# Kernel tuning notes

Hardware: AMD Instinct MI355X
Metric: run time of the kernel (lower is better)

The kernel has to match this reference:

```python
import jax, jax.numpy as jnp
import numpy as np

H, D_HEAD, MEM, K_OUT, J_DIM = 4, 16, 64, 192, 256
LN_EPS = 1e-5

def setup_inputs() -> dict:
    key = jax.random.key(0)
    ks = jax.random.split(key, 12)
    B, T, P = 4, 2048, 16
    inp = {
        "joint_repr": jax.random.normal(ks[0], (B, T, P, J_DIM), jnp.float32),
        "curvature": jax.random.uniform(ks[1], (B,), jnp.float32),
        "entropy": jax.random.uniform(ks[2], (B,), jnp.float32),
        "Wq": 0.02 * jax.random.normal(ks[3], (MEM, J_DIM), jnp.float32),
        "Wk": 0.02 * jax.random.normal(ks[4], (MEM, J_DIM), jnp.float32),
        "Wv": 0.02 * jax.random.normal(ks[5], (MEM, J_DIM), jnp.float32),
        "Wbeta_w": 0.05 * jax.random.normal(ks[6], (H, J_DIM), jnp.float32),
        "Wbeta_b": jnp.full((H,), 0.5, jnp.float32),
        "Walpha_w": 0.05 * jax.random.normal(ks[7], (H, J_DIM), jnp.float32),
        "Walpha_b": jnp.full((H,), -1.0, jnp.float32),
        "curv_w": 0.001 * jax.random.normal(ks[8], (H, 1), jnp.float32),
        "ent_w": 0.001 * jax.random.normal(ks[9], (H, 1), jnp.float32),
        "out_w": 0.01 * jax.random.normal(ks[10], (K_OUT, MEM), jnp.float32),
        "out_b": jnp.zeros((K_OUT,), jnp.float32),
        "ln_q_w": jnp.ones((D_HEAD,), jnp.float32),
        "ln_q_b": jnp.zeros((D_HEAD,), jnp.float32),
        "ln_k_w": jnp.ones((D_HEAD,), jnp.float32),
        "ln_k_b": jnp.zeros((D_HEAD,), jnp.float32),
    }
    return inp

def _ln(y, w, b):
    m = jnp.mean(y, axis=-1, keepdims=True)
    var = jnp.mean((y - m) ** 2, axis=-1, keepdims=True)
    return (y - m) / jnp.sqrt(var + LN_EPS) * w + b

def reference(joint_repr, curvature, entropy, Wq, Wk, Wv, Wbeta_w, Wbeta_b,
              Walpha_w, Walpha_b, curv_w, ent_w, out_w, out_b,
              ln_q_w, ln_q_b, ln_k_w, ln_k_b):
    B, T, P, J = joint_repr.shape
    N = B * P
    x = joint_repr.reshape(N, T, J)  # matches torch reshape(B*P, T, J)
    q = _ln((x @ Wq.T).reshape(N, T, H, D_HEAD), ln_q_w, ln_q_b)
    k = _ln((x @ Wk.T).reshape(N, T, H, D_HEAD), ln_k_w, ln_k_b)
    v = (x @ Wv.T).reshape(N, T, H, D_HEAD)
    k = k / jnp.clip(jnp.linalg.norm(k, axis=-1, keepdims=True), 1e-12)
    beta = jax.nn.sigmoid(x @ Wbeta_w.T + Wbeta_b)    # (N,T,H)
    alpha = jax.nn.sigmoid(x @ Walpha_w.T + Walpha_b)  # (N,T,H)
    # curvature modulation (detached in original)
    Kv = jnp.clip(jnp.abs(jax.lax.stop_gradient(curvature)), None, 10.0)
    Kv = jnp.repeat(Kv, P)  # (N,)
    beta = jax.nn.sigmoid(beta + Kv[:, None, None] * curv_w[:, 0])
    # entropy modulation (detached)
    Sv = jnp.clip(jax.lax.stop_gradient(entropy), 0.0, 5.0)
    Sv = jnp.repeat(Sv, P)
    alpha = jax.nn.sigmoid(alpha + Sv[:, None, None] * ent_w[:, 0])

    def step(M, inps):
        k_t, v_t, q_t, b_t, a_t = inps  # (N,H,d), (N,H)
        Mk = jnp.einsum('nhij,nhj->nhi', M, k_t)
        outer_kk = Mk[..., :, None] * k_t[..., None, :]
        outer_vk = v_t[..., :, None] * k_t[..., None, :]
        M = M - a_t[:, :, None, None] * outer_kk + b_t[:, :, None, None] * outer_vk
        o = jnp.einsum('nhij,nhj->nhi', M, q_t)
        return M, o

    M0 = jnp.zeros((N, H, D_HEAD, D_HEAD), joint_repr.dtype)
    xs = (k.transpose(1, 0, 2, 3), v.transpose(1, 0, 2, 3), q.transpose(1, 0, 2, 3),
          beta.transpose(1, 0, 2), alpha.transpose(1, 0, 2))
    _, outs = jax.lax.scan(step, M0, xs)  # (T,N,H,d)
    out = outs.transpose(1, 0, 2, 3).reshape(N, T, H * D_HEAD)
    fib = out @ out_w.T + out_b  # (N,T,K)
    return fib.reshape(B, P, T, K_OUT).transpose(0, 2, 1, 3)  # (B,T,P,K)
```

## Files before the change

### kernel.cpp

```cpp
#include <hip/hip_runtime.h>

#define TDIM 2048
#define SEG 16
#define SEGLEN 128

typedef __attribute__((ext_vector_type(8))) short short8;
typedef __attribute__((ext_vector_type(4))) short short4v;
typedef __attribute__((ext_vector_type(4))) float float4v;

__device__ __forceinline__ float sigf(float x) { return 1.0f / (1.0f + __expf(-x)); }

__device__ __forceinline__ unsigned short f2bf_rne(float f) {
    unsigned u = __float_as_uint(f);
    unsigned r = (u + 0x7fffu + ((u >> 16) & 1u)) >> 16;
    return (unsigned short)r;
}
__device__ __forceinline__ float bf2f(unsigned short h) {
    return __uint_as_float(((unsigned)h) << 16);
}
struct bfpair { short hi, lo; };
__device__ __forceinline__ bfpair cvt_split(float x) {
    bfpair p;
    unsigned short h = f2bf_rne(x);
    p.hi = (short)h;
    p.lo = (short)f2bf_rne(x - bf2f(h));
    return p;
}
__device__ __forceinline__ void split4(float4 v, short4v& hi, short4v& lo) {
    bfpair a = cvt_split(v.x), b = cvt_split(v.y), c = cvt_split(v.z), d = cvt_split(v.w);
    short4v h = {a.hi, b.hi, c.hi, d.hi};
    short4v l = {a.lo, b.lo, c.lo, d.lo};
    hi = h; lo = l;
}

#define RED16(v) { v += __shfl_xor(v, 1); v += __shfl_xor(v, 2); \
                   v += __shfl_xor(v, 4); v += __shfl_xor(v, 8); }

__device__ __forceinline__ float dot4f(float4 a, float4 b) {
    return fmaf(a.w, b.w, fmaf(a.z, b.z, fmaf(a.y, b.y, a.x * b.x)));
}
__device__ __forceinline__ float red4g(float v) {
    v += __shfl_xor(v, 16);
    v += __shfl_xor(v, 32);
    return v;
}

#define LROW 136

__global__ __launch_bounds__(256) void prep_w_kernel(
    const float* __restrict__ Wq, const float* __restrict__ Wk, const float* __restrict__ Wv,
    const float* __restrict__ Wbw, const float* __restrict__ Waw,
    short* __restrict__ wimg)
{
    int u = blockIdx.x * 256 + threadIdx.x;
    if (u >= 6656) return;
    int kc = u / 1664, rem = u % 1664;
    int rr = rem >> 3, gg = rem & 7;
    const float* wrow = nullptr;
    if (rr < 64)       wrow = Wq  + (size_t)rr * 256;
    else if (rr < 128) wrow = Wk  + (size_t)(rr - 64) * 256;
    else if (rr < 192) wrow = Wv  + (size_t)(rr - 128) * 256;
    else if (rr < 196) wrow = Wbw + (size_t)(rr - 192) * 256;
    else if (rr < 200) wrow = Waw + (size_t)(rr - 196) * 256;
    short* dst = wimg + (size_t)u * 16;
#pragma unroll
    for (int s = 0; s < 8; ++s) {
        float v = wrow ? wrow[kc * 64 + gg * 8 + s] : 0.0f;
        bfpair p = cvt_split(v);
        dst[s] = p.hi; dst[8 + s] = p.lo;
    }
}

__global__ __launch_bounds__(256) void prep_ow_kernel(
    const float* __restrict__ ow, short* __restrict__ owimg)
{
    int u = blockIdx.x * 256 + threadIdx.x;
    if (u >= 1536) return;
    int rr = u >> 3, gg = u & 7;
    short* dst = owimg + (size_t)u * 16;
#pragma unroll
    for (int s = 0; s < 8; ++s) {
        bfpair p = cvt_split(ow[(size_t)rr * 64 + gg * 8 + s]);
        dst[s] = p.hi; dst[8 + s] = p.lo;
    }
}

__global__ __launch_bounds__(256, 2) void proj_kernel(
    const float* __restrict__ x, const float* __restrict__ curv, const float* __restrict__ ent,
    const short* __restrict__ wimg,
    const float* __restrict__ Wbb, const float* __restrict__ Wab,
    const float* __restrict__ cw, const float* __restrict__ ew,
    const float* __restrict__ lnqw, const float* __restrict__ lnqb,
    const float* __restrict__ lnkw, const float* __restrict__ lnkb,
    float* __restrict__ q_ws, float* __restrict__ k_ws, float* __restrict__ v_ws,
    float* __restrict__ beta_ws, float* __restrict__ alpha_ws)
{
    __shared__ __align__(16) short xsh[64 * LROW];
    __shared__ __align__(16) short wsh[208 * LROW];

    const int tid = threadIdx.x;
    const int lane = tid & 63, wv = tid >> 6;
    const int row0 = blockIdx.x * 64;

    float4v acc[13];
#pragma unroll
    for (int cc = 0; cc < 13; ++cc) acc[cc] = (float4v){0.f, 0.f, 0.f, 0.f};

    for (int kc = 0; kc < 4; ++kc) {
        __syncthreads();
#pragma unroll
        for (int it = 0; it < 4; ++it) {
            int f = it * 256 + tid;
            int rr = f >> 4, c4 = f & 15;
            float4 xv = *(const float4*)&x[(size_t)(row0 + rr) * 256 + kc * 64 + c4 * 4];
            short4v hi, lo;
            split4(xv, hi, lo);
            short* ph = &xsh[rr * LROW + (c4 >> 1) * 16 + (c4 & 1) * 4];
            *(short4v*)ph = hi;
            *(short4v*)(ph + 8) = lo;
        }
        {
            const int4* wsrc = (const int4*)(wimg + (size_t)kc * 26624);
#pragma unroll
            for (int it = 0; it < 13; ++it) {
                int f = it * 256 + tid;
                int4 tv = wsrc[f];
                int row = f >> 4, idx = f & 15;
                *(int4*)&wsh[row * LROW + (idx >> 1) * 16 + (idx & 1) * 8] = tv;
            }
        }
        __syncthreads();
#pragma unroll
        for (int ks = 0; ks < 2; ++ks) {
            const int rowA = wv * 16 + (lane & 15);
            const int g4 = ks * 4 + (lane >> 4);
            short8 ah = *(const short8*)&xsh[rowA * LROW + g4 * 16];
            short8 al = *(const short8*)&xsh[rowA * LROW + g4 * 16 + 8];
#pragma unroll
            for (int nt = 0; nt < 13; ++nt) {
                const int rowB = nt * 16 + (lane & 15);
                short8 bh = *(const short8*)&wsh[rowB * LROW + g4 * 16];
                short8 bl = *(const short8*)&wsh[rowB * LROW + g4 * 16 + 8];
                acc[nt] = __builtin_amdgcn_mfma_f32_16x16x32_bf16(ah, bh, acc[nt], 0, 0, 0);
                acc[nt] = __builtin_amdgcn_mfma_f32_16x16x32_bf16(ah, bl, acc[nt], 0, 0, 0);
                acc[nt] = __builtin_amdgcn_mfma_f32_16x16x32_bf16(al, bh, acc[nt], 0, 0, 0);
            }
        }
    }

    const int c = lane & 15, lq = lane >> 4;
    const float lnqw_c = lnqw[c], lnqb_c = lnqb[c];
    const float lnkw_c = lnkw[c], lnkb_c = lnkb[c];
#pragma unroll
    for (int j = 0; j < 4; ++j) {
        const int grow = row0 + wv * 16 + lq * 4 + j;
        const int n = grow >> 11, t = grow & 2047;
#pragma unroll
        for (int h = 0; h < 4; ++h) {
            float y = acc[h][j];
            float s = y;  RED16(s);
            float s2 = y * y;  RED16(s2);
            float mean = s * 0.0625f;
            float var = s2 * 0.0625f - mean * mean;
            float inv = rsqrtf(var + 1e-5f);
            q_ws[((size_t)(n * 4 + h) * TDIM + t) * 16 + c] = (y - mean) * inv * lnqw_c + lnqb_c;
        }
#pragma unroll
        for (int h = 0; h < 4; ++h) {
            float y = acc[4 + h][j];
            float s = y;  RED16(s);
            float s2 = y * y;  RED16(s2);
            float mean = s * 0.0625f;
            float var = s2 * 0.0625f - mean * mean;
            float inv = rsqrtf(var + 1e-5f);
            float kn = (y - mean) * inv * lnkw_c + lnkb_c;
            float s3 = kn * kn;  RED16(s3);
            kn = kn / fmaxf(sqrtf(s3), 1e-12f);
            k_ws[((size_t)(n * 4 + h) * TDIM + t) * 16 + c] = kn;
        }
#pragma unroll
        for (int h = 0; h < 4; ++h)
            v_ws[((size_t)(n * 4 + h) * TDIM + t) * 16 + c] = acc[8 + h][j];
        float yb = acc[12][j];
        if (c < 4) {
            float Kv = fminf(fabsf(curv[n >> 4]), 10.0f);
            beta_ws[(size_t)(n * 4 + c) * TDIM + t] = sigf(sigf(yb + Wbb[c]) + Kv * cw[c]);
        } else if (c < 8) {
            int h = c - 4;
            float Sv = fminf(fmaxf(ent[n >> 4], 0.0f), 5.0f);
            alpha_ws[(size_t)(n * 4 + h) * TDIM + t] = sigf(sigf(yb + Wab[h]) + Sv * ew[h]);
        }
    }
}


__global__ __launch_bounds__(64) void scan_p1_kernel(
    const float* __restrict__ k_ws, const float* __restrict__ v_ws,
    const float* __restrict__ beta_ws, const float* __restrict__ alpha_ws,
    float* __restrict__ pq_ws)
{
    __shared__ __align__(16) float ks[128 * 16], bvs[128 * 16];
    __shared__ __align__(16) float tb1[128 * 4];
    const int tid = threadIdx.x;
    const int sid = blockIdx.x;
    const int cid = blockIdx.y;
    const int i = tid & 15, g = tid >> 4;
    const int t0g = sid * SEGLEN;
    const float* kb = k_ws + ((size_t)cid * TDIM + t0g) * 16;
    const float* vb = v_ws + ((size_t)cid * TDIM + t0g) * 16;
    const float* bb = beta_ws + (size_t)cid * TDIM + t0g;
    const float* ab = alpha_ws + (size_t)cid * TDIM + t0g;

    for (int f = tid; f < 128 * 16; f += 64) { ks[f] = 0.f; bvs[f] = 0.f; }
    for (int f = tid; f < 128 * 4; f += 64) tb1[f] = 0.f;
    __syncthreads();

    float4 kr[4], vr[4]; float be = 0.f, alp = 0.f;
    auto load_stage = [&](int s) {
        size_t t0 = (size_t)s * 64 + tid;
        const float4* kp = (const float4*)(kb + t0 * 16);
        const float4* vp = (const float4*)(vb + t0 * 16);
#pragma unroll
        for (int j = 0; j < 4; ++j) { kr[j] = kp[j]; vr[j] = vp[j]; }
        be = bb[t0]; alp = ab[t0];
    };
    auto commit_stage = [&](int s) {
        int r = (s & 1) * 64 + tid;
#pragma unroll
        for (int j = 0; j < 4; ++j) {
            *(float4*)&ks[r * 16 + 4 * j] = kr[j];
            float4 bv4 = make_float4(be * vr[j].x, be * vr[j].y, be * vr[j].z, be * vr[j].w);
            *(float4*)&bvs[r * 16 + 4 * j] = bv4;
        }
    };
    auto table_pass = [&](int s) {
        int r0 = (s & 1) * 64 + tid;
        int rm1 = (r0 - 1) & 127, rm2 = (r0 - 2) & 127;
        float C = 0.f, C2 = 0.f;
#pragma unroll
        for (int j = 0; j < 4; ++j) {
            float4 kt  = *(float4*)&ks[r0 * 16 + 4 * j];
            float4 km1 = *(float4*)&ks[rm1 * 16 + 4 * j];
            float4 km2 = *(float4*)&ks[rm2 * 16 + 4 * j];
            C  += dot4f(km1, kt);
            C2 += dot4f(km2, kt);
        }
        *(float4*)&tb1[r0 * 4] = make_float4(alp * C, alp * C2, alp, 0.f);
    };

    load_stage(0);
    commit_stage(0);
    __syncthreads();
    table_pass(0);
    __syncthreads();

    float4 Q4 = make_float4(0.f, 0.f, 0.f, 0.f);
    float4 P4 = make_float4(i == 4 * g + 0 ? 1.f : 0.f,
                            i == 4 * g + 1 ? 1.f : 0.f,
                            i == 4 * g + 2 ? 1.f : 0.f,
                            i == 4 * g + 3 ? 1.f : 0.f);
    float wq1 = 0.f, wq2 = 0.f, wp1 = 0.f, wp2 = 0.f;
    float4 k4m1 = make_float4(0.f, 0.f, 0.f, 0.f);
    float4 k4_0 = *(float4*)&ks[0 * 16 + 4 * g];
    float4 k4p1 = *(float4*)&ks[1 * 16 + 4 * g];
    float upQ_cur = 0.f;
    float upP_cur = ks[i];
    float4 ta0 = *(float4*)&tb1[0];
    float aC1_c = ta0.x, aC2_c = ta0.y, al_c = ta0.z;
    float bv_c = bvs[i];

    int t = 0;
    auto step = [&]() {
        int rp2 = (t + 2) & 127, rp1 = (t + 1) & 127;
        float4 k4in = *(float4*)&ks[rp2 * 16 + 4 * g];
        float4 tain = *(float4*)&tb1[rp1 * 4];
        float bvin = bvs[rp1 * 16 + i];
        float upQ = red4g(dot4f(Q4, k4p1));
        float upP = red4g(dot4f(P4, k4p1));
        Q4.x = fmaf(wq1, k4m1.x, Q4.x);
        Q4.y = fmaf(wq1, k4m1.y, Q4.y);
        Q4.z = fmaf(wq1, k4m1.z, Q4.z);
        Q4.w = fmaf(wq1, k4m1.w, Q4.w);
        P4.x = fmaf(wp1, k4m1.x, P4.x);
        P4.y = fmaf(wp1, k4m1.y, P4.y);
        P4.z = fmaf(wp1, k4m1.z, P4.z);
        P4.w = fmaf(wp1, k4m1.w, P4.w);
        float rq = fmaf(-aC2_c, wq2, fmaf(-al_c, upQ_cur, bv_c));
        float wq0 = fmaf(-aC1_c, wq1, rq);
        float rp_ = fmaf(-aC2_c, wp2, -al_c * upP_cur);
        float wp0 = fmaf(-aC1_c, wp1, rp_);
        wq2 = wq1; wq1 = wq0; wp2 = wp1; wp1 = wp0;
        k4m1 = k4_0; k4_0 = k4p1; k4p1 = k4in;
        upQ_cur = upQ; upP_cur = upP;
        aC1_c = tain.x; aC2_c = tain.y; al_c = tain.z; bv_c = bvin;
        ++t;
    };

    load_stage(1);
#pragma unroll 4
    for (int u = 0; u < 32; ++u) step();
    commit_stage(1);
#pragma unroll 4
    for (int u = 0; u < 16; ++u) step();
    table_pass(1);
#pragma unroll 4
    for (int u = 0; u < 16; ++u) step();
#pragma unroll 4
    for (int u = 0; u < 64; ++u) step();

    Q4.x = fmaf(wq1, k4m1.x, Q4.x);
    Q4.y = fmaf(wq1, k4m1.y, Q4.y);
    Q4.z = fmaf(wq1, k4m1.z, Q4.z);
    Q4.w = fmaf(wq1, k4m1.w, Q4.w);
    P4.x = fmaf(wp1, k4m1.x, P4.x);
    P4.y = fmaf(wp1, k4m1.y, P4.y);
    P4.z = fmaf(wp1, k4m1.z, P4.z);
    P4.w = fmaf(wp1, k4m1.w, P4.w);

    float* dst = pq_ws + ((size_t)cid * 15 + sid) * 512;
    *(float4*)&dst[i * 16 + 4 * g] = Q4;
    *(float4*)&dst[256 + i * 16 + 4 * g] = P4;
}

__global__ __launch_bounds__(64) void scan_p2_kernel(
    const float* __restrict__ pq_ws, float* __restrict__ min_ws)
{
    __shared__ float Mlds[256], Plds[256];
    const int tid = threadIdx.x;
    const int cid = blockIdx.x;
    const int i = tid & 15, g = tid >> 4;
    float4 M4 = make_float4(0.f, 0.f, 0.f, 0.f);
    *(float4*)&min_ws[((size_t)cid * SEG + 0) * 256 + i * 16 + 4 * g] = M4;
    for (int sid = 0; sid < 15; ++sid) {
        const float* base = pq_ws + ((size_t)cid * 15 + sid) * 512;
        float4 Qn = *(const float4*)&base[i * 16 + 4 * g];
        float4 Pn = *(const float4*)&base[256 + i * 16 + 4 * g];
        *(float4*)&Mlds[i * 16 + 4 * g] = M4;
        *(float4*)&Plds[i * 16 + 4 * g] = Pn;
        __syncthreads();
        float4 acc = Qn;
#pragma unroll
        for (int m = 0; m < 16; ++m) {
            float mm = Mlds[i * 16 + m];
            float4 pr = *(float4*)&Plds[m * 16 + 4 * g];
            acc.x = fmaf(mm, pr.x, acc.x);
            acc.y = fmaf(mm, pr.y, acc.y);
            acc.z = fmaf(mm, pr.z, acc.z);
            acc.w = fmaf(mm, pr.w, acc.w);
        }
        M4 = acc;
        __syncthreads();
        *(float4*)&min_ws[((size_t)cid * SEG + sid + 1) * 256 + i * 16 + 4 * g] = M4;
    }
}

__global__ __launch_bounds__(64) void scan_p3_kernel(
    const float* __restrict__ q_ws, const float* __restrict__ k_ws, const float* __restrict__ v_ws,
    const float* __restrict__ beta_ws, const float* __restrict__ alpha_ws,
    const float* __restrict__ min_ws, float* __restrict__ o_ws)
{
    __shared__ __align__(16) float ks[128 * 16], qs[128 * 16], bvs[128 * 16];
    __shared__ __align__(16) float tbl[128 * 8];
    __shared__ __align__(16) float os[64 * 16];
    const int tid = threadIdx.x;
    const int sid = blockIdx.x;
    const int cid = blockIdx.y;
    const int i = tid & 15, g = tid >> 4;
    const int t0g = sid * SEGLEN;
    const float* kb = k_ws + ((size_t)cid * TDIM + t0g) * 16;
    const float* qb = q_ws + ((size_t)cid * TDIM + t0g) * 16;
    const float* vb = v_ws + ((size_t)cid * TDIM + t0g) * 16;
    const float* bb = beta_ws + (size_t)cid * TDIM + t0g;
    const float* ab = alpha_ws + (size_t)cid * TDIM + t0g;
    float* obp = o_ws + ((size_t)cid * TDIM + t0g) * 16;

    for (int f = tid; f < 128 * 16; f += 64) { ks[f] = 0.f; qs[f] = 0.f; bvs[f] = 0.f; }
    for (int f = tid; f < 128 * 8; f += 64) tbl[f] = 0.f;
    __syncthreads();

    float4 kr[4], qr[4], vr[4]; float be = 0.f, alp = 0.f;
    auto load_stage = [&](int s) {
        size_t t0 = (size_t)s * 64 + tid;
        const float4* kp = (const float4*)(kb + t0 * 16);
        const float4* qp = (const float4*)(qb + t0 * 16);
        const float4* vp = (const float4*)(vb + t0 * 16);
#pragma unroll
        for (int j = 0; j < 4; ++j) { kr[j] = kp[j]; qr[j] = qp[j]; vr[j] = vp[j]; }
        be = bb[t0]; alp = ab[t0];
    };
    auto commit_stage = [&](int s) {
        int r = (s & 1) * 64 + tid;
#pragma unroll
        for (int j = 0; j < 4; ++j) {
            *(float4*)&ks[r * 16 + 4 * j] = kr[j];
            *(float4*)&qs[r * 16 + 4 * j] = qr[j];
            float4 bv4 = make_float4(be * vr[j].x, be * vr[j].y, be * vr[j].z, be * vr[j].w);
            *(float4*)&bvs[r * 16 + 4 * j] = bv4;
        }
    };
    auto table_pass = [&](int s) {
        int r0 = (s & 1) * 64 + tid;
        int rm1 = (r0 - 1) & 127, rm2 = (r0 - 2) & 127;
        float C = 0.f, C2 = 0.f, d = 0.f, e = 0.f, E2 = 0.f;
#pragma unroll
        for (int j = 0; j < 4; ++j) {
            float4 kt  = *(float4*)&ks[r0 * 16 + 4 * j];
            float4 km1 = *(float4*)&ks[rm1 * 16 + 4 * j];
            float4 km2 = *(float4*)&ks[rm2 * 16 + 4 * j];
            float4 qt  = *(float4*)&qs[r0 * 16 + 4 * j];
            C  += dot4f(km1, kt);
            C2 += dot4f(km2, kt);
            d  += dot4f(kt,  qt);
            e  += dot4f(km1, qt);
            E2 += dot4f(km2, qt);
        }
        *(float4*)&tbl[r0 * 8] = make_float4(alp * C, alp * C2, d, e);
        *(float2*)&tbl[r0 * 8 + 4] = make_float2(E2, alp);
    };

    load_stage(0);
    commit_stage(0);
    __syncthreads();
    table_pass(0);
    __syncthreads();

    float4 M4 = *(const float4*)&min_ws[((size_t)cid * SEG + sid) * 256 + i * 16 + 4 * g];
    float w1 = 0.f, w2 = 0.f;
    float4 k4m1 = make_float4(0.f, 0.f, 0.f, 0.f);
    float4 k4_0 = *(float4*)&ks[0 * 16 + 4 * g];
    float4 q4_0 = *(float4*)&qs[0 * 16 + 4 * g];
    float4 k4p1 = *(float4*)&ks[1 * 16 + 4 * g];
    float4 q4p1 = *(float4*)&qs[1 * 16 + 4 * g];
    float up_cur = red4g(dot4f(M4, k4_0));
    float rp_cur = red4g(dot4f(M4, q4_0));
    float4 ta0 = *(float4*)&tbl[0];
    float aC1_c = ta0.x, aC2_c = ta0.y, d_c = ta0.z, e_c = ta0.w;
    float2 tx0 = *(float2*)&tbl[4];
    float E2_c = tx0.x, al_c = tx0.y;
    float bv_c = bvs[i];

    int t = 0;
    auto step = [&]() {
        int rp2 = (t + 2) & 127, rp1 = (t + 1) & 127;
        float4 k4in = *(float4*)&ks[rp2 * 16 + 4 * g];
        float4 q4in = *(float4*)&qs[rp2 * 16 + 4 * g];
        float4 tain = *(float4*)&tbl[rp1 * 8];
        float2 txin = *(float2*)&tbl[rp1 * 8 + 4];
        float bvin = bvs[rp1 * 16 + i];
        float up = red4g(dot4f(M4, k4p1));
        float rp = red4g(dot4f(M4, q4p1));
        M4.x = fmaf(w1, k4m1.x, M4.x);
        M4.y = fmaf(w1, k4m1.y, M4.y);
        M4.z = fmaf(w1, k4m1.z, M4.z);
        M4.w = fmaf(w1, k4m1.w, M4.w);
        float r = fmaf(-aC2_c, w2, fmaf(-al_c, up_cur, bv_c));
        float w0 = fmaf(-aC1_c, w1, r);
        float o = fmaf(w0, d_c, fmaf(w1, e_c, fmaf(w2, E2_c, rp_cur)));
        if (g == 0) os[(t & 63) * 16 + i] = o;
        w2 = w1; w1 = w0;
        k4m1 = k4_0; k4_0 = k4p1; k4p1 = k4in;
        q4p1 = q4in;
        up_cur = up; rp_cur = rp;
        aC1_c = tain.x; aC2_c = tain.y; d_c = tain.z; e_c = tain.w;
        E2_c = txin.x; al_c = txin.y; bv_c = bvin;
        ++t;
    };

    for (int s = 0; s < 2; ++s) {
        if (s == 0) load_stage(1);
#pragma unroll 4
        for (int u = 0; u < 32; ++u) step();
        if (s == 0) commit_stage(1);
#pragma unroll 4
        for (int u = 0; u < 16; ++u) step();
        if (s == 0) table_pass(1);
#pragma unroll 4
        for (int u = 0; u < 16; ++u) step();
#pragma unroll
        for (int j = 0; j < 4; ++j) {
            float4 ov = *(float4*)&os[(tid * 4 + j) * 4];
            *(float4*)&obp[(size_t)s * 1024 + (tid * 4 + j) * 4] = ov;
        }
    }
}

__global__ __launch_bounds__(256, 2) void outproj_kernel(
    const float* __restrict__ o_ws, const short* __restrict__ owimg,
    const float* __restrict__ ob, float* __restrict__ out)
{
    __shared__ __align__(16) short osh[64 * LROW];
    __shared__ __align__(16) short wsh[192 * LROW];
    const int tid = threadIdx.x;
    const int lane = tid & 63, wv = tid >> 6;
    const int row0 = blockIdx.x * 64;

    float4v acc[12];
#pragma unroll
    for (int cc = 0; cc < 12; ++cc) acc[cc] = (float4v){0.f, 0.f, 0.f, 0.f};

#pragma unroll
    for (int it = 0; it < 4; ++it) {
        int f = it * 256 + tid;
        int rr = f >> 4, c4 = f & 15;
        int grow = row0 + rr;
        int n = grow >> 11, t = grow & 2047;
        int h = c4 >> 2, d4 = c4 & 3;
        float4 xv = *(const float4*)&o_ws[((size_t)(n * 4 + h) * TDIM + t) * 16 + d4 * 4];
        short4v hi, lo;
        split4(xv, hi, lo);
        short* ph = &osh[rr * LROW + (c4 >> 1) * 16 + (c4 & 1) * 4];
        *(short4v*)ph = hi;
        *(short4v*)(ph + 8) = lo;
    }
    {
        const int4* wsrc = (const int4*)owimg;
#pragma unroll
        for (int it = 0; it < 12; ++it) {
            int f = it * 256 + tid;
            int4 tv = wsrc[f];
            int row = f >> 4, idx = f & 15;
            *(int4*)&wsh[row * LROW + (idx >> 1) * 16 + (idx & 1) * 8] = tv;
        }
    }
    __syncthreads();

#pragma unroll
    for (int ks = 0; ks < 2; ++ks) {
        const int rowA = wv * 16 + (lane & 15);
        const int g4 = ks * 4 + (lane >> 4);
        short8 ah = *(const short8*)&osh[rowA * LROW + g4 * 16];
        short8 al = *(const short8*)&osh[rowA * LROW + g4 * 16 + 8];
#pragma unroll
        for (int nt = 0; nt < 12; ++nt) {
            const int rowB = nt * 16 + (lane & 15);
            short8 bh = *(const short8*)&wsh[rowB * LROW + g4 * 16];
            short8 bl = *(const short8*)&wsh[rowB * LROW + g4 * 16 + 8];
            acc[nt] = __builtin_amdgcn_mfma_f32_16x16x32_bf16(ah, bh, acc[nt], 0, 0, 0);
            acc[nt] = __builtin_amdgcn_mfma_f32_16x16x32_bf16(ah, bl, acc[nt], 0, 0, 0);
            acc[nt] = __builtin_amdgcn_mfma_f32_16x16x32_bf16(al, bh, acc[nt], 0, 0, 0);
        }
    }

    const int c = lane & 15, lq = lane >> 4;
#pragma unroll
    for (int nt = 0; nt < 12; ++nt) {
        float bias = ob[nt * 16 + c];
#pragma unroll
        for (int j = 0; j < 4; ++j) {
            int grow = row0 + wv * 16 + lq * 4 + j;
            int n = grow >> 11, t = grow & 2047;
            int b = n >> 4, p = n & 15;
            out[((size_t)(b * TDIM + t) * 16 + p) * 192 + nt * 16 + c] = acc[nt][j] + bias;
        }
    }
}

extern "C" void kernel_launch(void* const* d_in, const int* in_sizes, int n_in,
                              void* d_out, int out_size, void* d_ws, size_t ws_size,
                              hipStream_t stream) {
    (void)in_sizes; (void)n_in; (void)out_size; (void)ws_size;
    const float* x    = (const float*)d_in[0];
    const float* curv = (const float*)d_in[1];
    const float* ent  = (const float*)d_in[2];
    const float* Wq   = (const float*)d_in[3];
    const float* Wk   = (const float*)d_in[4];
    const float* Wv   = (const float*)d_in[5];
    const float* Wbw  = (const float*)d_in[6];
    const float* Wbb  = (const float*)d_in[7];
    const float* Waw  = (const float*)d_in[8];
    const float* Wab  = (const float*)d_in[9];
    const float* cw   = (const float*)d_in[10];
    const float* ew   = (const float*)d_in[11];
    const float* ow   = (const float*)d_in[12];
    const float* ob   = (const float*)d_in[13];
    const float* lnqw = (const float*)d_in[14];
    const float* lnqb = (const float*)d_in[15];
    const float* lnkw = (const float*)d_in[16];
    const float* lnkb = (const float*)d_in[17];
    float* out = (float*)d_out;

    float* ws = (float*)d_ws;
    float* q_ws     = ws;
    float* k_ws     = q_ws + 8388608;
    float* v_ws     = k_ws + 8388608;
    float* beta_ws  = v_ws + 8388608;
    float* alpha_ws = beta_ws + 524288;
    float* o_ws     = alpha_ws + 524288;

    short* wimg  = (short*)o_ws;
    short* owimg = (short*)q_ws;
    float* pq_ws  = out;
    float* min_ws = out + 1966080;

    prep_w_kernel<<<26, 256, 0, stream>>>(Wq, Wk, Wv, Wbw, Waw, wimg);
    proj_kernel<<<2048, 256, 0, stream>>>(x, curv, ent, wimg, Wbb, Wab,
                                          cw, ew, lnqw, lnqb, lnkw, lnkb,
                                          q_ws, k_ws, v_ws, beta_ws, alpha_ws);
    scan_p1_kernel<<<dim3(15, 256), 64, 0, stream>>>(k_ws, v_ws, beta_ws, alpha_ws, pq_ws);
    scan_p2_kernel<<<256, 64, 0, stream>>>(pq_ws, min_ws);
    scan_p3_kernel<<<dim3(16, 256), 64, 0, stream>>>(q_ws, k_ws, v_ws, beta_ws, alpha_ws,
                                                     min_ws, o_ws);
    prep_ow_kernel<<<6, 256, 0, stream>>>(ow, owimg);
    outproj_kernel<<<2048, 256, 0, stream>>>(o_ws, owimg, ob, out);
}
```

Before: 495.2 us.

## Restructure projection GEMMs with column-split waves, swizzled LDS, and direct global-to-LDS loads

The projection and output-projection GEMMs now split output columns across waves instead of rows, so each wave keeps A fragments for all 64 rows in registers and reuses them across its column tiles. LDS padding is replaced by an XOR swizzle baked into the prepacked weight images, and weights are copied with global_load_lds. The next x chunk is prefetched into registers while the current one is converted. Further changes are packed bf16 conversion via v_cvt_pk_bf16_f32 and DPP-based 16-lane reductions. These target LDS traffic, bank conflicts and load latency, at the cost of uneven work per wave (4 vs 3 tiles) and hand-written waitcnt handling.

```diff
diff --git a/kernel.cpp b/kernel.cpp
--- a/kernel.cpp
+++ b/kernel.cpp
@@ -26,15 +26,36 @@
     p.lo = (short)f2bf_rne(x - bf2f(h));
     return p;
 }
-__device__ __forceinline__ void split4(float4 v, short4v& hi, short4v& lo) {
-    bfpair a = cvt_split(v.x), b = cvt_split(v.y), c = cvt_split(v.z), d = cvt_split(v.w);
-    short4v h = {a.hi, b.hi, c.hi, d.hi};
-    short4v l = {a.lo, b.lo, c.lo, d.lo};
-    hi = h; lo = l;
-}
-
-#define RED16(v) { v += __shfl_xor(v, 1); v += __shfl_xor(v, 2); \
-                   v += __shfl_xor(v, 4); v += __shfl_xor(v, 8); }
+
+__device__ __forceinline__ void split4_fast(float4 v, short4v& hi, short4v& lo) {
+    unsigned h01, h23;
+    asm("v_cvt_pk_bf16_f32 %0, %1, %2" : "=v"(h01) : "v"(v.x), "v"(v.y));
+    asm("v_cvt_pk_bf16_f32 %0, %1, %2" : "=v"(h23) : "v"(v.z), "v"(v.w));
+    float rx = v.x - __uint_as_float(h01 << 16);
+    float ry = v.y - __uint_as_float(h01 & 0xffff0000u);
+    float rz = v.z - __uint_as_float(h23 << 16);
+    float rw = v.w - __uint_as_float(h23 & 0xffff0000u);
+    unsigned l01, l23;
+    asm("v_cvt_pk_bf16_f32 %0, %1, %2" : "=v"(l01) : "v"(rx), "v"(ry));
+    asm("v_cvt_pk_bf16_f32 %0, %1, %2" : "=v"(l23) : "v"(rz), "v"(rw));
+    union { unsigned u[2]; short4v s; } uh, ul;
+    uh.u[0] = h01; uh.u[1] = h23;
+    ul.u[0] = l01; ul.u[1] = l23;
+    hi = uh.s; lo = ul.s;
+}
+
+template<int CTRL>
+__device__ __forceinline__ float dpp_addt(float v) {
+    int t = __builtin_amdgcn_update_dpp(0, __float_as_int(v), CTRL, 0xf, 0xf, true);
+    return v + __int_as_float(t);
+}
+__device__ __forceinline__ float red16d(float v) {
+    v = dpp_addt<0xB1>(v);
+    v = dpp_addt<0x4E>(v);
+    v = dpp_addt<0x141>(v);
+    v = dpp_addt<0x140>(v);
+    return v;
+}
 
 __device__ __forceinline__ float dot4f(float4 a, float4 b) {
     return fmaf(a.w, b.w, fmaf(a.z, b.z, fmaf(a.y, b.y, a.x * b.x)));
@@ -45,7 +66,11 @@
     return v;
 }
 
-#define LROW 136
+__device__ __forceinline__ void gld16(const void* g, void* l) {
+    __builtin_amdgcn_global_load_lds(
+        (const __attribute__((address_space(1))) unsigned*)g,
+        (__attribute__((address_space(3))) unsigned*)l, 16, 0, 0);
+}
 
 __global__ __launch_bounds__(256) void prep_w_kernel(
     const float* __restrict__ Wq, const float* __restrict__ Wk, const float* __restrict__ Wv,
@@ -62,12 +87,14 @@
     else if (rr < 192) wrow = Wv  + (size_t)(rr - 128) * 256;
     else if (rr < 196) wrow = Wbw + (size_t)(rr - 192) * 256;
     else if (rr < 200) wrow = Waw + (size_t)(rr - 196) * 256;
-    short* dst = wimg + (size_t)u * 16;
+    int usw = (2 * gg) ^ (rr & 7);
+    short* dh = wimg + ((size_t)kc * 3328 + rr * 16 + usw) * 8;
+    short* dl = wimg + ((size_t)kc * 3328 + rr * 16 + (usw ^ 1)) * 8;
 #pragma unroll
     for (int s = 0; s < 8; ++s) {
         float v = wrow ? wrow[kc * 64 + gg * 8 + s] : 0.0f;
         bfpair p = cvt_split(v);
-        dst[s] = p.hi; dst[8 + s] = p.lo;
+        dh[s] = p.hi; dl[s] = p.lo;
     }
 }
 
@@ -77,11 +104,13 @@
     int u = blockIdx.x * 256 + threadIdx.x;
     if (u >= 1536) return;
     int rr = u >> 3, gg = u & 7;
-    short* dst = owimg + (size_t)u * 16;
+    int usw = (2 * gg) ^ (rr & 7);
+    short* dh = owimg + ((size_t)rr * 16 + usw) * 8;
+    short* dl = owimg + ((size_t)rr * 16 + (usw ^ 1)) * 8;
 #pragma unroll
     for (int s = 0; s < 8; ++s) {
         bfpair p = cvt_split(ow[(size_t)rr * 64 + gg * 8 + s]);
-        dst[s] = p.hi; dst[8 + s] = p.lo;
+        dh[s] = p.hi; dl[s] = p.lo;
     }
 }
 
@@ -95,104 +124,130 @@
     float* __restrict__ q_ws, float* __restrict__ k_ws, float* __restrict__ v_ws,
     float* __restrict__ beta_ws, float* __restrict__ alpha_ws)
 {
-    __shared__ __align__(16) short xsh[64 * LROW];
-    __shared__ __align__(16) short wsh[208 * LROW];
+    __shared__ __align__(16) short xsh[64 * 128];
+    __shared__ __align__(16) short wsh[208 * 128];
 
     const int tid = threadIdx.x;
     const int lane = tid & 63, wv = tid >> 6;
+    const int i16 = lane & 15, gq = lane >> 4, swz = i16 & 7;
     const int row0 = blockIdx.x * 64;
-
-    float4v acc[13];
-#pragma unroll
-    for (int cc = 0; cc < 13; ++cc) acc[cc] = (float4v){0.f, 0.f, 0.f, 0.f};
-
+    const int ntbase = (wv == 0) ? 0 : (1 + 3 * wv);
+    const int ntcnt  = (wv == 0) ? 4 : 3;
+
+    float4v acc[4][4];
+#pragma unroll
+    for (int m = 0; m < 4; ++m)
+#pragma unroll
+        for (int nI = 0; nI < 4; ++nI) acc[m][nI] = (float4v){0.f, 0.f, 0.f, 0.f};
+
+    float4 xr[4];
+#pragma unroll
+    for (int it = 0; it < 4; ++it) {
+        int f = it * 256 + tid, rr = f >> 4, c4 = f & 15;
+        xr[it] = *(const float4*)&x[(size_t)(row0 + rr) * 256 + c4 * 4];
+    }
+
+#pragma unroll
     for (int kc = 0; kc < 4; ++kc) {
-        __syncthreads();
+        __builtin_amdgcn_s_barrier();
+        const short* wsrc = wimg + (size_t)kc * 26624;
+#pragma unroll
+        for (int it = 0; it < 13; ++it) {
+            int f = it * 256 + tid;
+            gld16(wsrc + (size_t)f * 8, &wsh[f * 8]);
+        }
+        asm volatile("" ::: "memory");
 #pragma unroll
         for (int it = 0; it < 4; ++it) {
-            int f = it * 256 + tid;
-            int rr = f >> 4, c4 = f & 15;
-            float4 xv = *(const float4*)&x[(size_t)(row0 + rr) * 256 + kc * 64 + c4 * 4];
+            int f = it * 256 + tid, rr = f >> 4, c4 = f & 15;
             short4v hi, lo;
-            split4(xv, hi, lo);
-            short* ph = &xsh[rr * LROW + (c4 >> 1) * 16 + (c4 & 1) * 4];
-            *(short4v*)ph = hi;
-            *(short4v*)(ph + 8) = lo;
-        }
-        {
-            const int4* wsrc = (const int4*)(wimg + (size_t)kc * 26624);
-#pragma unroll
-            for (int it = 0; it < 13; ++it) {
-                int f = it * 256 + tid;
-                int4 tv = wsrc[f];
-                int row = f >> 4, idx = f & 15;
-                *(int4*)&wsh[row * LROW + (idx >> 1) * 16 + (idx & 1) * 8] = tv;
+            split4_fast(xr[it], hi, lo);
+            int usw = (2 * (c4 >> 1)) ^ (rr & 7);
+            *(short4v*)&xsh[rr * 128 + usw * 8 + (c4 & 1) * 4] = hi;
+            *(short4v*)&xsh[rr * 128 + (usw ^ 1) * 8 + (c4 & 1) * 4] = lo;
+        }
+        if (kc < 3) {
+#pragma unroll
+            for (int it = 0; it < 4; ++it) {
+                int f = it * 256 + tid, rr = f >> 4, c4 = f & 15;
+                xr[it] = *(const float4*)&x[(size_t)(row0 + rr) * 256 + (kc + 1) * 64 + c4 * 4];
             }
-        }
-        __syncthreads();
+            asm volatile("s_waitcnt vmcnt(4) lgkmcnt(0)" ::: "memory");
+        } else {
+            asm volatile("s_waitcnt vmcnt(0) lgkmcnt(0)" ::: "memory");
+        }
+        __builtin_amdgcn_s_barrier();
 #pragma unroll
         for (int ks = 0; ks < 2; ++ks) {
-            const int rowA = wv * 16 + (lane & 15);
-            const int g4 = ks * 4 + (lane >> 4);
-            short8 ah = *(const short8*)&xsh[rowA * LROW + g4 * 16];
-            short8 al = *(const short8*)&xsh[rowA * LROW + g4 * 16 + 8];
-#pragma unroll
-            for (int nt = 0; nt < 13; ++nt) {
-                const int rowB = nt * 16 + (lane & 15);
-                short8 bh = *(const short8*)&wsh[rowB * LROW + g4 * 16];
-                short8 bl = *(const short8*)&wsh[rowB * LROW + g4 * 16 + 8];
-                acc[nt] = __builtin_amdgcn_mfma_f32_16x16x32_bf16(ah, bh, acc[nt], 0, 0, 0);
-                acc[nt] = __builtin_amdgcn_mfma_f32_16x16x32_bf16(ah, bl, acc[nt], 0, 0, 0);
-                acc[nt] = __builtin_amdgcn_mfma_f32_16x16x32_bf16(al, bh, acc[nt], 0, 0, 0);
+            const int g4 = ks * 4 + gq;
+            const int uA = ((2 * g4) ^ swz) * 8;
+            short8 ah[4], al[4];
+#pragma unroll
+            for (int m = 0; m < 4; ++m) {
+                const int rb = (m * 16 + i16) * 128;
+                ah[m] = *(const short8*)&xsh[rb + uA];
+                al[m] = *(const short8*)&xsh[rb + (uA ^ 8)];
             }
-        }
-    }
-
-    const int c = lane & 15, lq = lane >> 4;
+#pragma unroll
+            for (int nI = 0; nI < 4; ++nI) if (nI < ntcnt) {
+                const int rowB = ((ntbase + nI) * 16 + i16) * 128;
+                short8 bh = *(const short8*)&wsh[rowB + uA];
+                short8 bl = *(const short8*)&wsh[rowB + (uA ^ 8)];
+#pragma unroll
+                for (int m = 0; m < 4; ++m) {
+                    acc[m][nI] = __builtin_amdgcn_mfma_f32_16x16x32_bf16(ah[m], bh, acc[m][nI], 0, 0, 0);
+                    acc[m][nI] = __builtin_amdgcn_mfma_f32_16x16x32_bf16(ah[m], bl, acc[m][nI], 0, 0, 0);
+                    acc[m][nI] = __builtin_amdgcn_mfma_f32_16x16x32_bf16(al[m], bh, acc[m][nI], 0, 0, 0);
+                }
+            }
+        }
+    }
+
+    const int c = i16;
     const float lnqw_c = lnqw[c], lnqb_c = lnqb[c];
     const float lnkw_c = lnkw[c], lnkb_c = lnkb[c];
-#pragma unroll
-    for (int j = 0; j < 4; ++j) {
-        const int grow = row0 + wv * 16 + lq * 4 + j;
-        const int n = grow >> 11, t = grow & 2047;
-#pragma unroll
-        for (int h = 0; h < 4; ++h) {
-            float y = acc[h][j];
-            float s = y;  RED16(s);
-            float s2 = y * y;  RED16(s2);
-            float mean = s * 0.0625f;
-            float var = s2 * 0.0625f - mean * mean;
-            float inv = rsqrtf(var + 1e-5f);
-            q_ws[((size_t)(n * 4 + h) * TDIM + t) * 16 + c] = (y - mean) * inv * lnqw_c + lnqb_c;
-        }
-#pragma unroll
-        for (int h = 0; h < 4; ++h) {
-            float y = acc[4 + h][j];
-            float s = y;  RED16(s);
-            float s2 = y * y;  RED16(s2);
-            float mean = s * 0.0625f;
-            float var = s2 * 0.0625f - mean * mean;
-            float inv = rsqrtf(var + 1e-5f);
-            float kn = (y - mean) * inv * lnkw_c + lnkb_c;
-            float s3 = kn * kn;  RED16(s3);
-            kn = kn / fmaxf(sqrtf(s3), 1e-12f);
-            k_ws[((size_t)(n * 4 + h) * TDIM + t) * 16 + c] = kn;
-        }
-#pragma unroll
-        for (int h = 0; h < 4; ++h)
-            v_ws[((size_t)(n * 4 + h) * TDIM + t) * 16 + c] = acc[8 + h][j];
-        float yb = acc[12][j];
-        if (c < 4) {
-            float Kv = fminf(fabsf(curv[n >> 4]), 10.0f);
-            beta_ws[(size_t)(n * 4 + c) * TDIM + t] = sigf(sigf(yb + Wbb[c]) + Kv * cw[c]);
-        } else if (c < 8) {
-            int h = c - 4;
-            float Sv = fminf(fmaxf(ent[n >> 4], 0.0f), 5.0f);
-            alpha_ws[(size_t)(n * 4 + h) * TDIM + t] = sigf(sigf(yb + Wab[h]) + Sv * ew[h]);
-        }
-    }
-}
-
+    const int nblk = row0 >> 11;
+    const float Kv = fminf(fabsf(curv[nblk >> 4]), 10.0f);
+    const float Sv = fminf(fmaxf(ent[nblk >> 4], 0.0f), 5.0f);
+#pragma unroll
+    for (int nI = 0; nI < 4; ++nI) if (nI < ntcnt) {
+        const int nt = ntbase + nI;
+#pragma unroll
+        for (int m = 0; m < 4; ++m) {
+#pragma unroll
+            for (int j = 0; j < 4; ++j) {
+                const int grow = row0 + m * 16 + gq * 4 + j;
+                const int n = grow >> 11, t = grow & 2047;
+                float y = acc[m][nI][j];
+                if (nt < 4) {
+                    float s = red16d(y), s2 = red16d(y * y);
+                    float mean = s * 0.0625f;
+                    float var = s2 * 0.0625f - mean * mean;
+                    float inv = rsqrtf(var + 1e-5f);
+                    q_ws[((size_t)(n * 4 + nt) * TDIM + t) * 16 + c] = (y - mean) * inv * lnqw_c + lnqb_c;
+                } else if (nt < 8) {
+                    float s = red16d(y), s2 = red16d(y * y);
+                    float mean = s * 0.0625f;
+                    float var = s2 * 0.0625f - mean * mean;
+                    float inv = rsqrtf(var + 1e-5f);
+                    float kn = (y - mean) * inv * lnkw_c + lnkb_c;
+                    float s3 = red16d(kn * kn);
+                    kn = kn / fmaxf(sqrtf(s3), 1e-12f);
+                    k_ws[((size_t)(n * 4 + (nt - 4)) * TDIM + t) * 16 + c] = kn;
+                } else if (nt < 12) {
+                    v_ws[((size_t)(n * 4 + (nt - 8)) * TDIM + t) * 16 + c] = y;
+                } else {
+                    if (c < 4)
+                        beta_ws[(size_t)(n * 4 + c) * TDIM + t] = sigf(sigf(y + Wbb[c]) + Kv * cw[c]);
+                    else if (c < 8) {
+                        int h = c - 4;
+                        alpha_ws[(size_t)(n * 4 + h) * TDIM + t] = sigf(sigf(y + Wab[h]) + Sv * ew[h]);
+                    }
+                }
+            }
+        }
+    }
+}
 
 __global__ __launch_bounds__(64) void scan_p1_kernel(
     const float* __restrict__ k_ws, const float* __restrict__ v_ws,
@@ -488,69 +543,79 @@
     const float* __restrict__ o_ws, const short* __restrict__ owimg,
     const float* __restrict__ ob, float* __restrict__ out)
 {
-    __shared__ __align__(16) short osh[64 * LROW];
-    __shared__ __align__(16) short wsh[192 * LROW];
+    __shared__ __align__(16) short osh[64 * 128];
+    __shared__ __align__(16) short wsh[192 * 128];
     const int tid = threadIdx.x;
     const int lane = tid & 63, wv = tid >> 6;
+    const int i16 = lane & 15, gq = lane >> 4, swz = i16 & 7;
     const int row0 = blockIdx.x * 64;
-
-    float4v acc[12];
-#pragma unroll
-    for (int cc = 0; cc < 12; ++cc) acc[cc] = (float4v){0.f, 0.f, 0.f, 0.f};
-
+    const int ntbase = wv * 3;
+
+    float4v acc[4][3];
+#pragma unroll
+    for (int m = 0; m < 4; ++m)
+#pragma unroll
+        for (int nI = 0; nI < 3; ++nI) acc[m][nI] = (float4v){0.f, 0.f, 0.f, 0.f};
+
+#pragma unroll
+    for (int it = 0; it < 12; ++it) {
+        int f = it * 256 + tid;
+        gld16(owimg + (size_t)f * 8, &wsh[f * 8]);
+    }
+    asm volatile("" ::: "memory");
 #pragma unroll
     for (int it = 0; it < 4; ++it) {
-        int f = it * 256 + tid;
-        int rr = f >> 4, c4 = f & 15;
+        int f = it * 256 + tid, rr = f >> 4, c4 = f & 15;
         int grow = row0 + rr;
         int n = grow >> 11, t = grow & 2047;
         int h = c4 >> 2, d4 = c4 & 3;
         float4 xv = *(const float4*)&o_ws[((size_t)(n * 4 + h) * TDIM + t) * 16 + d4 * 4];
         short4v hi, lo;
-        split4(xv, hi, lo);
-        short* ph = &osh[rr * LROW + (c4 >> 1) * 16 + (c4 & 1) * 4];
-        *(short4v*)ph = hi;
-        *(short4v*)(ph + 8) = lo;
-    }
-    {
-        const int4* wsrc = (const int4*)owimg;
-#pragma unroll
-        for (int it = 0; it < 12; ++it) {
-            int f = it * 256 + tid;
-            int4 tv = wsrc[f];
-            int row = f >> 4, idx = f & 15;
-            *(int4*)&wsh[row * LROW + (idx >> 1) * 16 + (idx & 1) * 8] = tv;
-        }
+        split4_fast(xv, hi, lo);
+        int usw = (2 * (c4 >> 1)) ^ (rr & 7);
+        *(short4v*)&osh[rr * 128 + usw * 8 + (c4 & 1) * 4] = hi;
+        *(short4v*)&osh[rr * 128 + (usw ^ 1) * 8 + (c4 & 1) * 4] = lo;
     }
     __syncthreads();
 
 #pragma unroll
     for (int ks = 0; ks < 2; ++ks) {
-        const int rowA = wv * 16 + (lane & 15);
-        const int g4 = ks * 4 + (lane >> 4);
-        short8 ah = *(const short8*)&osh[rowA * LROW + g4 * 16];
-        short8 al = *(const short8*)&osh[rowA * LROW + g4 * 16 + 8];
-#pragma unroll
-        for (int nt = 0; nt < 12; ++nt) {
-            const int rowB = nt * 16 + (lane & 15);
-            short8 bh = *(const short8*)&wsh[rowB * LROW + g4 * 16];
-            short8 bl = *(const short8*)&wsh[rowB * LROW + g4 * 16 + 8];
-            acc[nt] = __builtin_amdgcn_mfma_f32_16x16x32_bf16(ah, bh, acc[nt], 0, 0, 0);
-            acc[nt] = __builtin_amdgcn_mfma_f32_16x16x32_bf16(ah, bl, acc[nt], 0, 0, 0);
-            acc[nt] = __builtin_amdgcn_mfma_f32_16x16x32_bf16(al, bh, acc[nt], 0, 0, 0);
-        }
-    }
-
-    const int c = lane & 15, lq = lane >> 4;
-#pragma unroll
-    for (int nt = 0; nt < 12; ++nt) {
-        float bias = ob[nt * 16 + c];
-#pragma unroll
-        for (int j = 0; j < 4; ++j) {
-            int grow = row0 + wv * 16 + lq * 4 + j;
-            int n = grow >> 11, t = grow & 2047;
-            int b = n >> 4, p = n & 15;
-            out[((size_t)(b * TDIM + t) * 16 + p) * 192 + nt * 16 + c] = acc[nt][j] + bias;
+        const int g4 = ks * 4 + gq;
+        const int uA = ((2 * g4) ^ swz) * 8;
+        short8 ah[4], al[4];
+#pragma unroll
+        for (int m = 0; m < 4; ++m) {
+            const int rb = (m * 16 + i16) * 128;
+            ah[m] = *(const short8*)&osh[rb + uA];
+            al[m] = *(const short8*)&osh[rb + (uA ^ 8)];
+        }
+#pragma unroll
+        for (int nI = 0; nI < 3; ++nI) {
+            const int rowB = ((ntbase + nI) * 16 + i16) * 128;
+            short8 bh = *(const short8*)&wsh[rowB + uA];
+            short8 bl = *(const short8*)&wsh[rowB + (uA ^ 8)];
+#pragma unroll
+            for (int m = 0; m < 4; ++m) {
+                acc[m][nI] = __builtin_amdgcn_mfma_f32_16x16x32_bf16(ah[m], bh, acc[m][nI], 0, 0, 0);
+                acc[m][nI] = __builtin_amdgcn_mfma_f32_16x16x32_bf16(ah[m], bl, acc[m][nI], 0, 0, 0);
+                acc[m][nI] = __builtin_amdgcn_mfma_f32_16x16x32_bf16(al[m], bh, acc[m][nI], 0, 0, 0);
+            }
+        }
+    }
+
+#pragma unroll
+    for (int nI = 0; nI < 3; ++nI) {
+        const int nt = ntbase + nI;
+        const float bias = ob[nt * 16 + i16];
+#pragma unroll
+        for (int m = 0; m < 4; ++m) {
+#pragma unroll
+            for (int j = 0; j < 4; ++j) {
+                int grow = row0 + m * 16 + gq * 4 + j;
+                int n = grow >> 11, t = grow & 2047;
+                int b = n >> 4, p = n & 15;
+                out[((size_t)(b * TDIM + t) * 16 + p) * 192 + nt * 16 + i16] = acc[m][nI][j] + bias;
+            }
         }
     }
 }
```

Result: slower. 512.9 us (+3.6%).
